# Kernel tuning notes

Measured on AMD Instinct MI355X. Metric: run time of the kernel, lower is better.

Reference implementation:

```python
import jax, jax.numpy as jnp
import numpy as np
import math

B, L, S, E, D = 32, 2048, 2048, 64, 64

def setup_inputs() -> dict:
    key = jax.random.key(0)
    kq, kk, kv = jax.random.split(key, 3)
    return {
        "queries": jax.random.normal(kq, (B, L, E), dtype=jnp.float32),
        "keys":    jax.random.normal(kk, (B, S, E), dtype=jnp.float32),
        "values":  jax.random.normal(kv, (B, S, D), dtype=jnp.float32),
    }

def reference(queries, keys, values):
    # scale = 1/sqrt(E) since self.scale is None
    scale = 1.0 / math.sqrt(queries.shape[-1])
    # unfused QK^T -> softmax -> V (dropout is identity at inference)
    scores = jnp.einsum('ble,bse->bls', queries, keys)  # [B,L,S]
    # mask_flag branch not taken because L == S (matches torch code path)
    A = jax.nn.softmax(scale * scores, axis=-1)
    V = jnp.einsum('bls,bsd->bld', A, values)  # [B,L,D]
    return V
```

## Files before the change

kernel.cpp:

```cpp
#include <hip/hip_runtime.h>
#include <hip/hip_bf16.h>


#define B_ 32
#define L_ 2048
#define S_ 2048
#define E_ 64
#define D_ 64
#define BQ 128
#define NIMG 32
#define IMG_BYTES 16384
#define NCHUNK 16

typedef __attribute__((ext_vector_type(8))) short bf16x8;
typedef __attribute__((ext_vector_type(16))) float f32x16;
typedef __attribute__((ext_vector_type(4))) unsigned u32x4;

__device__ __forceinline__ unsigned short f2b(float f) {
  unsigned u = __builtin_bit_cast(unsigned, f);
  u += 0x7fff + ((u >> 16) & 1);
  return (unsigned short)(u >> 16);
}

__device__ __forceinline__ unsigned pk2(float a, float b) {
#if defined(__has_builtin) && __has_builtin(__builtin_amdgcn_cvt_pk_bf16_f32)
  typedef __bf16 b2 __attribute__((ext_vector_type(2)));
  b2 t = __builtin_amdgcn_cvt_pk_bf16_f32(a, b);
  return __builtin_bit_cast(unsigned, t);
#else
  return (unsigned)f2b(a) | ((unsigned)f2b(b) << 16);
#endif
}

__device__ __forceinline__ float fexp2(float x) {
#if defined(__has_builtin) && __has_builtin(__builtin_amdgcn_exp2f)
  return __builtin_amdgcn_exp2f(x);
#else
  return exp2f(x);
#endif
}

__device__ __forceinline__ void cp16(const void* g, void* lbase) {
#if defined(__has_builtin) && __has_builtin(__builtin_amdgcn_global_load_lds)
  typedef const __attribute__((address_space(1))) void gvoid;
  typedef __attribute__((address_space(3))) void lvoid;
  __builtin_amdgcn_global_load_lds((gvoid*)g, (lvoid*)lbase, 16, 0, 0);
#endif
}

__global__ __launch_bounds__(256) void prepass(
    const float* __restrict__ K, const float* __restrict__ V,
    char* __restrict__ ws) {
  const int tid  = threadIdx.x;
  const int lane = tid & 63;
  const int quad = lane >> 4;
  const int qb0  = quad & 1;
  const int qb1  = (quad >> 1) & 1;

  const int b  = blockIdx.x >> 5;
  const int c  = blockIdx.x & 31;
  const int s0 = c * 64;

  const float* Kb = K + (long)b * S_ * E_;
  const float* Vb = V + (long)b * S_ * D_;
  short* img = (short*)(ws + (size_t)blockIdx.x * IMG_BYTES);

#pragma unroll
  for (int it = 0; it < 4; ++it) {
    const int i  = tid + it * 256;
    const int s  = i >> 4;
    const int c4 = (i & 15) << 2;

    float4 kv = *(const float4*)(Kb + (long)(s0 + s) * E_ + c4);
    {
      int g = ((c4 >> 3) + s) & 7;
      *(uint2*)&img[s * 64 + g * 8 + (c4 & 7)] = make_uint2(pk2(kv.x, kv.y), pk2(kv.z, kv.w));
    }

    float4 vv = *(const float4*)(Vb + (long)(s0 + s) * D_ + c4);
    float a0 = vv.x, a1 = vv.y, a2 = vv.z, a3 = vv.w;
    float s0f = qb1 ? a0 : a2;
    float s1f = qb1 ? a1 : a3;
    float r0  = __shfl_xor(s0f, 32);
    float r1  = __shfl_xor(s1f, 32);
    float b0 = qb1 ? r0 : a0;
    float b1 = qb1 ? r1 : a1;
    float b2 = qb1 ? a2 : r0;
    float b3 = qb1 ? a3 : r1;
    float t0 = qb0 ? b0 : b1;
    float t1 = qb0 ? b2 : b3;
    float u0 = __shfl_xor(t0, 16);
    float u1 = __shfl_xor(t1, 16);
    float w0 = qb0 ? u0 : b0;
    float w1 = qb0 ? b1 : u0;
    float w2 = qb0 ? u1 : b2;
    float w3 = qb0 ? b3 : u1;
    const int base = s - quad;
    const int d    = c4 + quad;
    int g = ((base >> 3) + d) & 7;
    *(uint2*)&img[4096 + d * 64 + g * 8 + (base & 7)] = make_uint2(pk2(w0, w1), pk2(w2, w3));
  }
}

__global__ __launch_bounds__(512, 4) void attn_fwd(
    const float* __restrict__ Q, const char* __restrict__ ws,
    float* __restrict__ O) {
  __shared__ __align__(16) char smem[65536 + 1024];
  float* Obuf = (float*)smem;
  float* ML   = (float*)(smem + 65536);

  const int tid  = threadIdx.x;
  const int lane = tid & 63;
  const int wv   = tid >> 6;
  const int l31  = lane & 31;
  const int h    = lane >> 5;
  const int qg   = wv >> 1;
  const int kh   = wv & 1;

  const int b  = blockIdx.x >> 4;
  const int q0 = (blockIdx.x & 15) * BQ;

  const float SCALE2 = 0.125f * 1.44269504088896340736f;
  const char* img0 = ws + (size_t)b * ((size_t)NIMG * IMG_BYTES);

#pragma unroll
  for (int j = 0; j < 4; ++j)
    cp16(img0 + wv * 4096 + j * 1024 + lane * 16, smem + wv * 4096 + j * 1024);

  bf16x8 qf[4];
  {
    const float* qrow = Q + ((long)b * L_ + q0 + qg * 32 + l31) * E_;
#pragma unroll
    for (int ke = 0; ke < 4; ++ke) {
      const float* sp = qrow + ke * 16 + h * 8;
      float4 x = *(const float4*)(sp);
      float4 y = *(const float4*)(sp + 4);
      u32x4 uu = { pk2(x.x * SCALE2, x.y * SCALE2), pk2(x.z * SCALE2, x.w * SCALE2),
                   pk2(y.x * SCALE2, y.y * SCALE2), pk2(y.z * SCALE2, y.w * SCALE2) };
      qf[ke] = __builtin_bit_cast(bf16x8, uu);
    }
  }

  int offK[2][4];
#pragma unroll
  for (int nt = 0; nt < 2; ++nt) {
    const int row = nt * 32 + l31;
#pragma unroll
    for (int ke = 0; ke < 4; ++ke)
      offK[nt][ke] = kh * 16384 + row * 128 + (((ke * 2 + h) + row) & 7) * 16;
  }
  int offV[2][4];
#pragma unroll
  for (int mt = 0; mt < 2; ++mt) {
    const int d = mt * 32 + l31;
#pragma unroll
    for (int ks = 0; ks < 4; ++ks)
      offV[mt][ks] = kh * 16384 + 8192 + d * 128 + (((ks * 2 + h) + d) & 7) * 16;
  }

  f32x16 o[2];
#pragma unroll
  for (int mt = 0; mt < 2; ++mt)
#pragma unroll
    for (int r = 0; r < 16; ++r) o[mt][r] = 0.f;
  float lrun = 0.f;

  __syncthreads();

#define CHUNK_BODY(TT, BUFB, OTHB)                                              \
  {                                                                             \
    if ((TT) + 1 < NCHUNK) {                                                    \
      const char* img = img0 + (size_t)((TT) + 1) * 32768;                      \
      _Pragma("unroll")                                                         \
      for (int j = 0; j < 4; ++j)                                               \
        cp16(img + wv * 4096 + j * 1024 + lane * 16,                            \
             smem + (OTHB) + wv * 4096 + j * 1024);                             \
    }                                                                           \
    bf16x8 pf[2][2];                                                            \
    _Pragma("unroll")                                                           \
    for (int nt = 0; nt < 2; ++nt) {                                            \
      bf16x8 kf[4];                                                             \
      _Pragma("unroll")                                                         \
      for (int ke = 0; ke < 4; ++ke)                                            \
        kf[ke] = *(const bf16x8*)(smem + (BUFB) + offK[nt][ke]);                \
      f32x16 acc;                                                               \
      _Pragma("unroll")                                                         \
      for (int r = 0; r < 16; ++r) acc[r] = 0.f;                                \
      _Pragma("unroll")                                                         \
      for (int ke = 0; ke < 4; ++ke)                                            \
        acc = __builtin_amdgcn_mfma_f32_32x32x16_bf16(kf[ke], qf[ke], acc,      \
                                                      0, 0, 0);                 \
      float pr[16];                                                             \
      float rs = 0.f;                                                           \
      _Pragma("unroll")                                                         \
      for (int r = 0; r < 16; ++r) {                                            \
        pr[r] = fexp2(acc[r]);                                                  \
        rs += pr[r];                                                            \
      }                                                                         \
      lrun += rs;                                                               \
      unsigned u[4][2];                                                         \
      _Pragma("unroll")                                                         \
      for (int g = 0; g < 4; ++g) {                                             \
        u[g][0] = pk2(pr[4 * g + 0], pr[4 * g + 1]);                            \
        u[g][1] = pk2(pr[4 * g + 2], pr[4 * g + 3]);                            \
      }                                                                         \
      unsigned sa0 = h ? u[0][0] : u[1][0];                                     \
      unsigned sa1 = h ? u[0][1] : u[1][1];                                     \
      unsigned ra0 = (unsigned)__shfl_xor((int)sa0, 32);                        \
      unsigned ra1 = (unsigned)__shfl_xor((int)sa1, 32);                        \
      u32x4 f0 = { h ? ra0 : u[0][0], h ? ra1 : u[0][1],                        \
                   h ? u[1][0] : ra0, h ? u[1][1] : ra1 };                      \
      pf[nt][0] = __builtin_bit_cast(bf16x8, f0);                               \
      unsigned sb0 = h ? u[2][0] : u[3][0];                                     \
      unsigned sb1 = h ? u[2][1] : u[3][1];                                     \
      unsigned rb0 = (unsigned)__shfl_xor((int)sb0, 32);                        \
      unsigned rb1 = (unsigned)__shfl_xor((int)sb1, 32);                        \
      u32x4 f1 = { h ? rb0 : u[2][0], h ? rb1 : u[2][1],                        \
                   h ? u[3][0] : rb0, h ? u[3][1] : rb1 };                      \
      pf[nt][1] = __builtin_bit_cast(bf16x8, f1);                               \
    }                                                                           \
    _Pragma("unroll")                                                           \
    for (int mt = 0; mt < 2; ++mt) {                                            \
      _Pragma("unroll")                                                         \
      for (int ks = 0; ks < 4; ++ks) {                                          \
        bf16x8 vf = *(const bf16x8*)(smem + (BUFB) + offV[mt][ks]);             \
        o[mt] = __builtin_amdgcn_mfma_f32_32x32x16_bf16(vf, pf[ks >> 1][ks & 1],\
                                                        o[mt], 0, 0, 0);        \
      }                                                                         \
    }                                                                           \
    __syncthreads();                                                            \
  }

  for (int t = 0; t < NCHUNK; t += 2) {
    CHUNK_BODY(t, 0, 32768)
    CHUNK_BODY(t + 1, 32768, 0)
  }
#undef CHUNK_BODY

  float lt = lrun + __shfl_xor(lrun, 32);

  if (lane < 32)
    ML[(qg * 2 + kh) * 32 + l31] = lt;
  __syncthreads();

  const float inv = 1.f / (lt + ML[(qg * 2 + (kh ^ 1)) * 32 + l31]);
  const int q = qg * 32 + l31;

  if (kh == 1) {
#pragma unroll
    for (int mt = 0; mt < 2; ++mt)
#pragma unroll
      for (int r = 0; r < 16; ++r) {
        const int d = mt * 32 + (r & 3) + 8 * (r >> 2) + 4 * h;
        Obuf[q * 68 + d] = o[mt][r];
      }
  }
  __syncthreads();

  if (kh == 0) {
#pragma unroll
    for (int mt = 0; mt < 2; ++mt)
#pragma unroll
      for (int r = 0; r < 16; ++r) {
        const int d = mt * 32 + (r & 3) + 8 * (r >> 2) + 4 * h;
        Obuf[q * 68 + d] = (o[mt][r] + Obuf[q * 68 + d]) * inv;
      }
  }
  __syncthreads();

  {
    const int qq = tid >> 2;
    const int dh = (tid & 3) * 16;
    float* orow = O + ((long)b * L_ + q0 + qq) * D_ + dh;
    const float* src = &Obuf[qq * 68 + dh];
#pragma unroll
    for (int j = 0; j < 4; ++j)
      *(float4*)(orow + j * 4) = *(const float4*)(src + j * 4);
  }
}

extern "C" void kernel_launch(void* const* d_in, const int* in_sizes, int n_in,
                              void* d_out, int out_size, void* d_ws, size_t ws_size,
                              hipStream_t stream) {
  const float* Q = (const float*)d_in[0];
  const float* K = (const float*)d_in[1];
  const float* V = (const float*)d_in[2];
  float* O = (float*)d_out;

  prepass<<<dim3(B_ * NIMG), dim3(256), 0, stream>>>(K, V, (char*)d_ws);
  attn_fwd<<<dim3(B_ * (L_ / BQ)), dim3(512), 0, stream>>>(Q, (const char*)d_ws, O);
}
```

Before: 143.4 us.

## Read K/V fragments directly from global in MFMA-ready layout, drop LDS staging

The prepass now writes K and V images in a per-lane fragment order, so each lane can fetch its MFMA operand as one contiguous 16-byte global load. The attention kernel drops the double-buffered LDS staging and the per-chunk barriers. Each block now handles 32 queries with 4 waves, and each wave covers a quarter of the key range. Partial outputs and row sums are combined through a small LDS buffer at the end. This removes LDS traffic and synchronisation but relies on L2/cache for K/V reuse, since there is no overlap of global loads with compute. Each block now fetches the full K/V for only 32 queries, which multiplies global/L2 traffic.

```diff
diff --git a/kernel.cpp b/kernel.cpp
--- a/kernel.cpp
+++ b/kernel.cpp
@@ -7,10 +7,9 @@
 #define S_ 2048
 #define E_ 64
 #define D_ 64
-#define BQ 128
+#define BQ 32
 #define NIMG 32
 #define IMG_BYTES 16384
-#define NCHUNK 16
 
 typedef __attribute__((ext_vector_type(8))) short bf16x8;
 typedef __attribute__((ext_vector_type(16))) float f32x16;
@@ -40,14 +39,6 @@
 #endif
 }
 
-__device__ __forceinline__ void cp16(const void* g, void* lbase) {
-#if defined(__has_builtin) && __has_builtin(__builtin_amdgcn_global_load_lds)
-  typedef const __attribute__((address_space(1))) void gvoid;
-  typedef __attribute__((address_space(3))) void lvoid;
-  __builtin_amdgcn_global_load_lds((gvoid*)g, (lvoid*)lbase, 16, 0, 0);
-#endif
-}
-
 __global__ __launch_bounds__(256) void prepass(
     const float* __restrict__ K, const float* __restrict__ V,
     char* __restrict__ ws) {
@@ -73,8 +64,11 @@
 
     float4 kv = *(const float4*)(Kb + (long)(s0 + s) * E_ + c4);
     {
-      int g = ((c4 >> 3) + s) & 7;
-      *(uint2*)&img[s * 64 + g * 8 + (c4 & 7)] = make_uint2(pk2(kv.x, kv.y), pk2(kv.z, kv.w));
+      const int bk   = (s >> 5) * 4 + (c4 >> 4);
+      const int ln   = ((c4 >> 3) & 1) * 32 + (s & 31);
+      const int half = (c4 >> 2) & 1;
+      *(uint2*)&img[bk * 512 + ln * 8 + half * 4] =
+          make_uint2(pk2(kv.x, kv.y), pk2(kv.z, kv.w));
     }
 
     float4 vv = *(const float4*)(Vb + (long)(s0 + s) * D_ + c4);
@@ -97,39 +91,38 @@
     float w3 = qb0 ? b3 : u1;
     const int base = s - quad;
     const int d    = c4 + quad;
-    int g = ((base >> 3) + d) & 7;
-    *(uint2*)&img[4096 + d * 64 + g * 8 + (base & 7)] = make_uint2(pk2(w0, w1), pk2(w2, w3));
-  }
-}
-
-__global__ __launch_bounds__(512, 4) void attn_fwd(
+    {
+      const int bv   = (d >> 5) * 4 + (base >> 4);
+      const int ln   = ((base >> 3) & 1) * 32 + (d & 31);
+      const int half = (base >> 2) & 1;
+      *(uint2*)&img[4096 + bv * 512 + ln * 8 + half * 4] =
+          make_uint2(pk2(w0, w1), pk2(w2, w3));
+    }
+  }
+}
+
+__global__ __launch_bounds__(256, 5) void attn_fwd(
     const float* __restrict__ Q, const char* __restrict__ ws,
     float* __restrict__ O) {
-  __shared__ __align__(16) char smem[65536 + 1024];
-  float* Obuf = (float*)smem;
-  float* ML   = (float*)(smem + 65536);
+  __shared__ float Obuf[BQ * 68];
+  __shared__ float Lbuf[4 * BQ];
 
   const int tid  = threadIdx.x;
   const int lane = tid & 63;
   const int wv   = tid >> 6;
   const int l31  = lane & 31;
   const int h    = lane >> 5;
-  const int qg   = wv >> 1;
-  const int kh   = wv & 1;
-
-  const int b  = blockIdx.x >> 4;
-  const int q0 = (blockIdx.x & 15) * BQ;
+
+  const int b  = blockIdx.x >> 6;
+  const int q0 = (blockIdx.x & 63) * BQ;
 
   const float SCALE2 = 0.125f * 1.44269504088896340736f;
   const char* img0 = ws + (size_t)b * ((size_t)NIMG * IMG_BYTES);
-
-#pragma unroll
-  for (int j = 0; j < 4; ++j)
-    cp16(img0 + wv * 4096 + j * 1024 + lane * 16, smem + wv * 4096 + j * 1024);
+  const int wvs = __builtin_amdgcn_readfirstlane(wv);
 
   bf16x8 qf[4];
   {
-    const float* qrow = Q + ((long)b * L_ + q0 + qg * 32 + l31) * E_;
+    const float* qrow = Q + ((long)b * L_ + q0 + l31) * E_;
 #pragma unroll
     for (int ke = 0; ke < 4; ++ke) {
       const float* sp = qrow + ke * 16 + h * 8;
@@ -141,23 +134,6 @@
     }
   }
 
-  int offK[2][4];
-#pragma unroll
-  for (int nt = 0; nt < 2; ++nt) {
-    const int row = nt * 32 + l31;
-#pragma unroll
-    for (int ke = 0; ke < 4; ++ke)
-      offK[nt][ke] = kh * 16384 + row * 128 + (((ke * 2 + h) + row) & 7) * 16;
-  }
-  int offV[2][4];
-#pragma unroll
-  for (int mt = 0; mt < 2; ++mt) {
-    const int d = mt * 32 + l31;
-#pragma unroll
-    for (int ks = 0; ks < 4; ++ks)
-      offV[mt][ks] = kh * 16384 + 8192 + d * 128 + (((ks * 2 + h) + d) & 7) * 16;
-  }
-
   f32x16 o[2];
 #pragma unroll
   for (int mt = 0; mt < 2; ++mt)
@@ -165,117 +141,96 @@
     for (int r = 0; r < 16; ++r) o[mt][r] = 0.f;
   float lrun = 0.f;
 
+  const int lb = lane * 16;
+
+  for (int i = 0; i < 8; ++i) {
+    const char* img = img0 + (size_t)(wvs + i * 4) * IMG_BYTES;
+
+    bf16x8 pf[2][2];
+#pragma unroll
+    for (int nt = 0; nt < 2; ++nt) {
+      bf16x8 kf[4];
+#pragma unroll
+      for (int ke = 0; ke < 4; ++ke)
+        kf[ke] = *(const bf16x8*)(img + (nt * 4 + ke) * 1024 + lb);
+      f32x16 acc;
+#pragma unroll
+      for (int r = 0; r < 16; ++r) acc[r] = 0.f;
+#pragma unroll
+      for (int ke = 0; ke < 4; ++ke)
+        acc = __builtin_amdgcn_mfma_f32_32x32x16_bf16(kf[ke], qf[ke], acc, 0, 0, 0);
+
+      float pr[16];
+      float rs = 0.f;
+#pragma unroll
+      for (int r = 0; r < 16; ++r) {
+        pr[r] = fexp2(acc[r]);
+        rs += pr[r];
+      }
+      lrun += rs;
+
+      unsigned u[4][2];
+#pragma unroll
+      for (int g = 0; g < 4; ++g) {
+        u[g][0] = pk2(pr[4 * g + 0], pr[4 * g + 1]);
+        u[g][1] = pk2(pr[4 * g + 2], pr[4 * g + 3]);
+      }
+      unsigned sa0 = h ? u[0][0] : u[1][0];
+      unsigned sa1 = h ? u[0][1] : u[1][1];
+      unsigned ra0 = (unsigned)__shfl_xor((int)sa0, 32);
+      unsigned ra1 = (unsigned)__shfl_xor((int)sa1, 32);
+      u32x4 f0 = { h ? ra0 : u[0][0], h ? ra1 : u[0][1],
+                   h ? u[1][0] : ra0, h ? u[1][1] : ra1 };
+      pf[nt][0] = __builtin_bit_cast(bf16x8, f0);
+      unsigned sb0 = h ? u[2][0] : u[3][0];
+      unsigned sb1 = h ? u[2][1] : u[3][1];
+      unsigned rb0 = (unsigned)__shfl_xor((int)sb0, 32);
+      unsigned rb1 = (unsigned)__shfl_xor((int)sb1, 32);
+      u32x4 f1 = { h ? rb0 : u[2][0], h ? rb1 : u[2][1],
+                   h ? u[3][0] : rb0, h ? u[3][1] : rb1 };
+      pf[nt][1] = __builtin_bit_cast(bf16x8, f1);
+    }
+
+#pragma unroll
+    for (int mt = 0; mt < 2; ++mt) {
+#pragma unroll
+      for (int ks = 0; ks < 4; ++ks) {
+        bf16x8 vf = *(const bf16x8*)(img + 8192 + (mt * 4 + ks) * 1024 + lb);
+        o[mt] = __builtin_amdgcn_mfma_f32_32x32x16_bf16(vf, pf[ks >> 1][ks & 1],
+                                                        o[mt], 0, 0, 0);
+      }
+    }
+  }
+
+  const float lt = lrun + __shfl_xor(lrun, 32);
+  Lbuf[wv * BQ + l31] = lt;
+
+#pragma unroll
+  for (int w = 0; w < 4; ++w) {
+    __syncthreads();
+    if (wv == w) {
+#pragma unroll
+      for (int mt = 0; mt < 2; ++mt)
+#pragma unroll
+        for (int r = 0; r < 16; ++r) {
+          const int d = mt * 32 + (r & 3) + 8 * (r >> 2) + 4 * h;
+          if (w == 0) Obuf[l31 * 68 + d] = o[mt][r];
+          else        Obuf[l31 * 68 + d] += o[mt][r];
+        }
+    }
+  }
   __syncthreads();
 
-#define CHUNK_BODY(TT, BUFB, OTHB)                                              \
-  {                                                                             \
-    if ((TT) + 1 < NCHUNK) {                                                    \
-      const char* img = img0 + (size_t)((TT) + 1) * 32768;                      \
-      _Pragma("unroll")                                                         \
-      for (int j = 0; j < 4; ++j)                                               \
-        cp16(img + wv * 4096 + j * 1024 + lane * 16,                            \
-             smem + (OTHB) + wv * 4096 + j * 1024);                             \
-    }                                                                           \
-    bf16x8 pf[2][2];                                                            \
-    _Pragma("unroll")                                                           \
-    for (int nt = 0; nt < 2; ++nt) {                                            \
-      bf16x8 kf[4];                                                             \
-      _Pragma("unroll")                                                         \
-      for (int ke = 0; ke < 4; ++ke)                                            \
-        kf[ke] = *(const bf16x8*)(smem + (BUFB) + offK[nt][ke]);                \
-      f32x16 acc;                                                               \
-      _Pragma("unroll")                                                         \
-      for (int r = 0; r < 16; ++r) acc[r] = 0.f;                                \
-      _Pragma("unroll")                                                         \
-      for (int ke = 0; ke < 4; ++ke)                                            \
-        acc = __builtin_amdgcn_mfma_f32_32x32x16_bf16(kf[ke], qf[ke], acc,      \
-                                                      0, 0, 0);                 \
-      float pr[16];                                                             \
-      float rs = 0.f;                                                           \
-      _Pragma("unroll")                                                         \
-      for (int r = 0; r < 16; ++r) {                                            \
-        pr[r] = fexp2(acc[r]);                                                  \
-        rs += pr[r];                                                            \
-      }                                                                         \
-      lrun += rs;                                                               \
-      unsigned u[4][2];                                                         \
-      _Pragma("unroll")                                                         \
-      for (int g = 0; g < 4; ++g) {                                             \
-        u[g][0] = pk2(pr[4 * g + 0], pr[4 * g + 1]);                            \
-        u[g][1] = pk2(pr[4 * g + 2], pr[4 * g + 3]);                            \
-      }                                                                         \
-      unsigned sa0 = h ? u[0][0] : u[1][0];                                     \
-      unsigned sa1 = h ? u[0][1] : u[1][1];                                     \
-      unsigned ra0 = (unsigned)__shfl_xor((int)sa0, 32);                        \
-      unsigned ra1 = (unsigned)__shfl_xor((int)sa1, 32);                        \
-      u32x4 f0 = { h ? ra0 : u[0][0], h ? ra1 : u[0][1],                        \
-                   h ? u[1][0] : ra0, h ? u[1][1] : ra1 };                      \
-      pf[nt][0] = __builtin_bit_cast(bf16x8, f0);                               \
-      unsigned sb0 = h ? u[2][0] : u[3][0];                                     \
-      unsigned sb1 = h ? u[2][1] : u[3][1];                                     \
-      unsigned rb0 = (unsigned)__shfl_xor((int)sb0, 32);                        \
-      unsigned rb1 = (unsigned)__shfl_xor((int)sb1, 32);                        \
-      u32x4 f1 = { h ? rb0 : u[2][0], h ? rb1 : u[2][1],                        \
-                   h ? u[3][0] : rb0, h ? u[3][1] : rb1 };                      \
-      pf[nt][1] = __builtin_bit_cast(bf16x8, f1);                               \
-    }                                                                           \
-    _Pragma("unroll")                                                           \
-    for (int mt = 0; mt < 2; ++mt) {                                            \
-      _Pragma("unroll")                                                         \
-      for (int ks = 0; ks < 4; ++ks) {                                          \
-        bf16x8 vf = *(const bf16x8*)(smem + (BUFB) + offV[mt][ks]);             \
-        o[mt] = __builtin_amdgcn_mfma_f32_32x32x16_bf16(vf, pf[ks >> 1][ks & 1],\
-                                                        o[mt], 0, 0, 0);        \
-      }                                                                         \
-    }                                                                           \
-    __syncthreads();                                                            \
-  }
-
-  for (int t = 0; t < NCHUNK; t += 2) {
-    CHUNK_BODY(t, 0, 32768)
-    CHUNK_BODY(t + 1, 32768, 0)
-  }
-#undef CHUNK_BODY
-
-  float lt = lrun + __shfl_xor(lrun, 32);
-
-  if (lane < 32)
-    ML[(qg * 2 + kh) * 32 + l31] = lt;
-  __syncthreads();
-
-  const float inv = 1.f / (lt + ML[(qg * 2 + (kh ^ 1)) * 32 + l31]);
-  const int q = qg * 32 + l31;
-
-  if (kh == 1) {
-#pragma unroll
-    for (int mt = 0; mt < 2; ++mt)
-#pragma unroll
-      for (int r = 0; r < 16; ++r) {
-        const int d = mt * 32 + (r & 3) + 8 * (r >> 2) + 4 * h;
-        Obuf[q * 68 + d] = o[mt][r];
-      }
-  }
-  __syncthreads();
-
-  if (kh == 0) {
-#pragma unroll
-    for (int mt = 0; mt < 2; ++mt)
-#pragma unroll
-      for (int r = 0; r < 16; ++r) {
-        const int d = mt * 32 + (r & 3) + 8 * (r >> 2) + 4 * h;
-        Obuf[q * 68 + d] = (o[mt][r] + Obuf[q * 68 + d]) * inv;
-      }
-  }
-  __syncthreads();
-
   {
-    const int qq = tid >> 2;
-    const int dh = (tid & 3) * 16;
-    float* orow = O + ((long)b * L_ + q0 + qq) * D_ + dh;
-    const float* src = &Obuf[qq * 68 + dh];
-#pragma unroll
-    for (int j = 0; j < 4; ++j)
-      *(float4*)(orow + j * 4) = *(const float4*)(src + j * 4);
+    const int q  = tid >> 3;
+    const int dg = (tid & 7) * 8;
+    const float inv = 1.f / (Lbuf[q] + Lbuf[BQ + q] + Lbuf[2 * BQ + q] + Lbuf[3 * BQ + q]);
+    float* orow = O + ((long)b * L_ + q0 + q) * D_ + dg;
+    const float* src = &Obuf[q * 68 + dg];
+    float4 v0 = { src[0] * inv, src[1] * inv, src[2] * inv, src[3] * inv };
+    float4 v1 = { src[4] * inv, src[5] * inv, src[6] * inv, src[7] * inv };
+    *(float4*)(orow)     = v0;
+    *(float4*)(orow + 4) = v1;
   }
 }
 
@@ -288,5 +243,5 @@
   float* O = (float*)d_out;
 
   prepass<<<dim3(B_ * NIMG), dim3(256), 0, stream>>>(K, V, (char*)d_ws);
-  attn_fwd<<<dim3(B_ * (L_ / BQ)), dim3(512), 0, stream>>>(Q, (const char*)d_ws, O);
-}
+  attn_fwd<<<dim3(B_ * (L_ / BQ)), dim3(256), 0, stream>>>(Q, (const char*)d_ws, O);
+}
```

New measurement: 183.8 us. +28.2%, slower.
